# Optimization experiments

Hardware: AMD Instinct MI355X
Metric: run time of the kernel (lower is better)

## Reference

```python
import jax, jax.numpy as jnp
import numpy as np

# Dimensions: B sequences, T max length, K tagset size
B, T, K = 512, 512, 128
START_TAG_IDX, END_TAG_IDX = 126, 127
NEG = -10000.0  # matches torch.full(..., -10000)


def setup_inputs() -> dict:
    key = jax.random.key(0)
    k1, k2, k3 = jax.random.split(key, 3)
    feats = jax.random.normal(k1, (B, T, K), dtype=jnp.float32)
    trans = jax.random.normal(k2, (K, K), dtype=jnp.float32)
    # __init__ clamps illegal transitions: into START, out of END
    trans = trans.at[:, START_TAG_IDX].set(NEG)
    trans = trans.at[END_TAG_IDX, :].set(NEG)
    # pack_sequence requires length-descending order; lengths in [1, T]
    lengths = jnp.sort(jax.random.randint(k3, (B,), 1, T + 1))[::-1].astype(jnp.int32)
    return {"feats": feats, "trans": trans, "lengths": lengths}


def reference(feats, trans, lengths):
    # CRF log-partition (score_z): forward algorithm over a padded batch.
    # Equivalent to the packed-sequence loop: at step t only sequences with
    # t < length update alpha; others keep their previous alpha.
    Bq, Tq, Kq = feats.shape
    alpha0 = jnp.full((Bq, Kq), NEG, dtype=feats.dtype).at[:, START_TAG_IDX].set(0.0)
    feats_t = jnp.swapaxes(feats, 0, 1)                       # [T,B,K]
    mask = jnp.arange(Tq, dtype=lengths.dtype)[:, None] < lengths[None, :]  # [T,B]

    def step(alpha, inp):
        f, m = inp  # f: [B,K] emissions, m: [B] legal mask
        # score[b,i,j] = feat[b,j] + alpha[b,i] + trans[i,j]
        score = f[:, None, :] + alpha[:, :, None] + trans[None, :, :]  # [B,K,K]
        alpha_new = jax.nn.logsumexp(score, axis=1)                    # [B,K]
        return jnp.where(m[:, None], alpha_new, alpha), None

    alpha, _ = jax.lax.scan(step, alpha0, (feats_t, mask))
    final = alpha + trans[:, END_TAG_IDX][None, :]
    return jnp.sum(jax.nn.logsumexp(final, axis=1))
```

## Files before the change

### kernel.cpp

```cpp
#include <hip/hip_runtime.h>

#define K_TAGS 128
#define T_MAX  512
#define N_SEQ  512
#define START_TAG 126
#define END_TAG   127
#define LOG2E 1.44269504088896340736f
#define LN2   0.69314718055994530942f

typedef float v2f __attribute__((ext_vector_type(2)));

__device__ __forceinline__ float fexp2(float x) { return exp2f(x); }
__device__ __forceinline__ float flog2(float x) { return __log2f(x); }

template <int CTRL>
__device__ __forceinline__ float dpp_swap(float x) {
  return __int_as_float(__builtin_amdgcn_update_dpp(
      0, __float_as_int(x), CTRL, 0xF, 0xF, true));
}

__device__ __forceinline__ void lds_barrier() {
  asm volatile("s_waitcnt lgkmcnt(0)" ::: "memory");
  __builtin_amdgcn_s_barrier();
  asm volatile("" ::: "memory");
}

__global__ __launch_bounds__(256, 2) void crf_fwd_kernel(
    const float* __restrict__ feats,
    const float* __restrict__ trans,
    const int*   __restrict__ lengths,
    float*       __restrict__ partial)
{
  const int blk = blockIdx.x;
  const int b   = (blk < N_SEQ / 2) ? blk : (3 * N_SEQ / 2 - 1 - blk);
  const int tid = (int)threadIdx.x;
  const int jg  = tid >> 2;
  const int q   = tid & 3;
  const int j0  = jg;
  const int j1  = jg + 64;
  const int i0  = q * 32;

  const int len = lengths[b];
  const float* fb = feats + (size_t)b * (T_MAX * K_TAGS);

  __shared__ __align__(16) float p_sh[2][K_TAGS];
  __shared__ float nrm[2];
  __shared__ float red[8];

  v2f E0[16], E1[16];
#pragma unroll
  for (int c = 0; c < 8; ++c) {
    const int r = i0 + 4 * (c ^ (q << 1));
    E0[2 * c + 0] = v2f{fexp2(trans[(r + 0) * K_TAGS + j0] * LOG2E),
                        fexp2(trans[(r + 1) * K_TAGS + j0] * LOG2E)};
    E0[2 * c + 1] = v2f{fexp2(trans[(r + 2) * K_TAGS + j0] * LOG2E),
                        fexp2(trans[(r + 3) * K_TAGS + j0] * LOG2E)};
    E1[2 * c + 0] = v2f{fexp2(trans[(r + 0) * K_TAGS + j1] * LOG2E),
                        fexp2(trans[(r + 1) * K_TAGS + j1] * LOG2E)};
    E1[2 * c + 1] = v2f{fexp2(trans[(r + 2) * K_TAGS + j1] * LOG2E),
                        fexp2(trans[(r + 3) * K_TAGS + j1] * LOG2E)};
  }

  if (q == 0) {
    p_sh[0][j0] = (j0 == START_TAG) ? 1.0f : 0.0f;
    p_sh[0][j1] = (j1 == START_TAG) ? 1.0f : 0.0f;
  }
  if (tid == 0) nrm[0] = 0.0f;

  float a0 = (j0 == START_TAG) ? 0.0f : -10000.0f * LOG2E;
  float a1 = (j1 == START_TAG) ? 0.0f : -10000.0f * LOG2E;
  float Ncur = 0.0f;

  float f0cur = fb[j0];
  float f1cur = fb[j1];
  const int t1 = (len > 1) ? 1 : 0;
  float f0nx = fb[t1 * K_TAGS + j0];
  float f1nx = fb[t1 * K_TAGS + j1];

#define STEP(BUF, TT)                                                        \
  {                                                                          \
    const int tp = ((TT) + 2 < len) ? ((TT) + 2) : (len - 1);                \
    const float nf0 = fb[tp * K_TAGS + j0];                                  \
    const float nf1 = fb[tp * K_TAGS + j1];                                  \
    lds_barrier();                                                           \
    const float Nnxt = nrm[BUF];                                             \
    const float d  = Ncur - Nnxt;                                            \
    const float g0 = fexp2(fmaf(f0cur, LOG2E, d));                           \
    const float g1 = fexp2(fmaf(f1cur, LOG2E, d));                           \
    const float* pp = p_sh[BUF];                                             \
    v2f s0a = {0.f, 0.f}, s0b = {0.f, 0.f};                                  \
    v2f s1a = {0.f, 0.f}, s1b = {0.f, 0.f};                                  \
    _Pragma("unroll")                                                        \
    for (int c = 0; c < 8; ++c) {                                            \
      const int w0 = i0 + 4 * (c ^ (q << 1));                                \
      const float4 pv = *reinterpret_cast<const float4*>(pp + w0);           \
      const v2f pA = {pv.x, pv.y};                                           \
      const v2f pB = {pv.z, pv.w};                                           \
      s0a = __builtin_elementwise_fma(pA, E0[2 * c + 0], s0a);               \
      s0b = __builtin_elementwise_fma(pB, E0[2 * c + 1], s0b);               \
      s1a = __builtin_elementwise_fma(pA, E1[2 * c + 0], s1a);               \
      s1b = __builtin_elementwise_fma(pB, E1[2 * c + 1], s1b);               \
    }                                                                        \
    const v2f s0 = s0a + s0b;                                                \
    const v2f s1 = s1a + s1b;                                                \
    float acc0 = s0.x + s0.y;                                                \
    float acc1 = s1.x + s1.y;                                                \
    acc0 += dpp_swap<0xB1>(acc0);                                            \
    acc0 += dpp_swap<0x4E>(acc0);                                            \
    acc1 += dpp_swap<0xB1>(acc1);                                            \
    acc1 += dpp_swap<0x4E>(acc1);                                            \
    const float p0 = acc0 * g0;                                              \
    const float p1 = acc1 * g1;                                              \
    if (q < 2) p_sh[(BUF) ^ 1][(q == 0) ? j0 : j1] = (q == 0) ? p0 : p1;     \
    a0 = fmaf(f0cur, LOG2E, Ncur + flog2(acc0));                             \
    a1 = fmaf(f1cur, LOG2E, Ncur + flog2(acc1));                             \
    if (tid == 0) nrm[(BUF) ^ 1] = a0;                                       \
    Ncur = Nnxt;                                                             \
    f0cur = f0nx; f1cur = f1nx;                                              \
    f0nx = nf0;   f1nx = nf1;                                                \
  }

  int t = 0;
  for (; t + 2 <= len; t += 2) {
    STEP(0, t)
    STEP(1, t + 1)
  }
  if (t < len) STEP(0, t)
#undef STEP

  __syncthreads();

  const float fin0 = a0 + trans[j0 * K_TAGS + END_TAG] * LOG2E;
  const float fin1 = a1 + trans[j1 * K_TAGS + END_TAG] * LOG2E;

  float m = fmaxf(fin0, fin1);
#pragma unroll
  for (int off = 4; off < 64; off <<= 1)
    m = fmaxf(m, __shfl_xor(m, off, 64));
  if ((tid & 63) == 0) red[tid >> 6] = m;
  __syncthreads();
  const float Mf = fmaxf(fmaxf(red[0], red[1]), fmaxf(red[2], red[3]));

  float e = (q == 0) ? (fexp2(fin0 - Mf) + fexp2(fin1 - Mf)) : 0.0f;
#pragma unroll
  for (int off = 1; off < 64; off <<= 1)
    e += __shfl_xor(e, off, 64);
  if ((tid & 63) == 0) red[4 + (tid >> 6)] = e;
  __syncthreads();
  if (tid == 0) {
    const float s = (red[4] + red[5]) + (red[6] + red[7]);
    partial[b] = (Mf + flog2(s)) * LN2;
  }
}

__global__ void crf_reduce(const float* __restrict__ partial,
                           float* __restrict__ out) {
  const int tid = (int)threadIdx.x;
  float s = partial[tid] + partial[tid + 256];
#pragma unroll
  for (int off = 1; off < 64; off <<= 1) s += __shfl_xor(s, off, 64);
  __shared__ float ws[4];
  if ((tid & 63) == 0) ws[tid >> 6] = s;
  __syncthreads();
  if (tid == 0) out[0] = (ws[0] + ws[1]) + (ws[2] + ws[3]);
}

extern "C" void kernel_launch(void* const* d_in, const int* in_sizes, int n_in,
                              void* d_out, int out_size, void* d_ws, size_t ws_size,
                              hipStream_t stream) {
  const float* feats   = (const float*)d_in[0];
  const float* trans   = (const float*)d_in[1];
  const int*   lengths = (const int*)d_in[2];
  float* partial = (float*)d_ws;
  float* out     = (float*)d_out;

  crf_fwd_kernel<<<dim3(N_SEQ), dim3(256), 0, stream>>>(feats, trans, lengths, partial);
  crf_reduce<<<dim3(1), dim3(256), 0, stream>>>(partial, out);
}
```

Baseline: 335.7 us.

## Renormalize CRF probabilities every two steps via block max, drop per-step log

Replaces the per-step log-domain normalization, which computed a log2 of the accumulator and broadcast one alpha through LDS, with a probability-domain recurrence. The running probabilities are rescaled every other step by the block-wide max, gathered through a 16-entry LDS reduction, and the log of that scale is accumulated into a scalar. Feature prefetch is deepened to four steps, and raw amdgcn exp2/log builtins are used. This removes transcendentals and a dependency from the serial critical path, at the cost of relying on the values staying in float range across two unnormalized steps.

```diff
diff --git a/kernel.cpp b/kernel.cpp
--- a/kernel.cpp
+++ b/kernel.cpp
@@ -10,11 +10,23 @@
 
 typedef float v2f __attribute__((ext_vector_type(2)));
 
-__device__ __forceinline__ float fexp2(float x) { return exp2f(x); }
-__device__ __forceinline__ float flog2(float x) { return __log2f(x); }
+__device__ __forceinline__ float fexp2(float x) {
+#if __has_builtin(__builtin_amdgcn_exp2f)
+  return __builtin_amdgcn_exp2f(x);
+#else
+  return exp2f(x);
+#endif
+}
+__device__ __forceinline__ float flog2(float x) {
+#if __has_builtin(__builtin_amdgcn_logf)
+  return __builtin_amdgcn_logf(x);
+#else
+  return __log2f(x);
+#endif
+}
 
 template <int CTRL>
-__device__ __forceinline__ float dpp_swap(float x) {
+__device__ __forceinline__ float dpp_mov(float x) {
   return __int_as_float(__builtin_amdgcn_update_dpp(
       0, __float_as_int(x), CTRL, 0xF, 0xF, true));
 }
@@ -44,8 +56,8 @@
   const float* fb = feats + (size_t)b * (T_MAX * K_TAGS);
 
   __shared__ __align__(16) float p_sh[2][K_TAGS];
-  __shared__ float nrm[2];
-  __shared__ float red[8];
+  __shared__ __align__(16) float red16[16];
+  __shared__ float red8[8];
 
   v2f E0[16], E1[16];
 #pragma unroll
@@ -65,28 +77,41 @@
     p_sh[0][j0] = (j0 == START_TAG) ? 1.0f : 0.0f;
     p_sh[0][j1] = (j1 == START_TAG) ? 1.0f : 0.0f;
   }
-  if (tid == 0) nrm[0] = 0.0f;
-
-  float a0 = (j0 == START_TAG) ? 0.0f : -10000.0f * LOG2E;
-  float a1 = (j1 == START_TAG) ? 0.0f : -10000.0f * LOG2E;
-  float Ncur = 0.0f;
-
-  float f0cur = fb[j0];
-  float f1cur = fb[j1];
-  const int t1 = (len > 1) ? 1 : 0;
-  float f0nx = fb[t1 * K_TAGS + j0];
-  float f1nx = fb[t1 * K_TAGS + j1];
-
-#define STEP(BUF, TT)                                                        \
+
+  float Cc  = 0.0f;
+  float pc0 = 0.0f, pc1 = 0.0f;
+
+  float fA0, fA1, fB0, fB1, fC0, fC1, fD0, fD1;
+  {
+    const int tB = (len > 1) ? 1 : 0;
+    const int tC = (len > 2) ? 2 : (len - 1);
+    const int tD = (len > 3) ? 3 : (len - 1);
+    fA0 = fb[j0];                fA1 = fb[j1];
+    fB0 = fb[tB * K_TAGS + j0];  fB1 = fb[tB * K_TAGS + j1];
+    fC0 = fb[tC * K_TAGS + j0];  fC1 = fb[tC * K_TAGS + j1];
+    fD0 = fb[tD * K_TAGS + j0];  fD1 = fb[tD * K_TAGS + j1];
+  }
+
+#define BODY(BUF, F0, F1, ODD, TT)                                           \
   {                                                                          \
-    const int tp = ((TT) + 2 < len) ? ((TT) + 2) : (len - 1);                \
-    const float nf0 = fb[tp * K_TAGS + j0];                                  \
-    const float nf1 = fb[tp * K_TAGS + j1];                                  \
+    const float fl0 = F0, fl1 = F1;      \
+    const int tp = ((TT) + 4 < len) ? ((TT) + 4) : (len - 1);                \
+    F0 = fb[tp * K_TAGS + j0];    \
+    F1 = fb[tp * K_TAGS + j1];                                               \
     lds_barrier();                                                           \
-    const float Nnxt = nrm[BUF];                                             \
-    const float d  = Ncur - Nnxt;                                            \
-    const float g0 = fexp2(fmaf(f0cur, LOG2E, d));                           \
-    const float g1 = fexp2(fmaf(f1cur, LOG2E, d));                           \
+    float D = 0.0f;                                                          \
+    if (ODD) {     \
+      const float4 r0 = *reinterpret_cast<const float4*>(&red16[0]);         \
+      const float4 r1 = *reinterpret_cast<const float4*>(&red16[4]);         \
+      const float4 r2 = *reinterpret_cast<const float4*>(&red16[8]);         \
+      const float4 r3 = *reinterpret_cast<const float4*>(&red16[12]);        \
+      float mm = fmaxf(fmaxf(fmaxf(r0.x, r0.y), fmaxf(r0.z, r0.w)),          \
+                       fmaxf(fmaxf(r1.x, r1.y), fmaxf(r1.z, r1.w)));         \
+      mm = fmaxf(mm, fmaxf(fmaxf(fmaxf(r2.x, r2.y), fmaxf(r2.z, r2.w)),     \
+                           fmaxf(fmaxf(r3.x, r3.y), fmaxf(r3.z, r3.w))));   \
+      D = flog2(mm);                                                         \
+      Cc += D;                                                               \
+    }                                                                        \
     const float* pp = p_sh[BUF];                                             \
     v2f s0a = {0.f, 0.f}, s0b = {0.f, 0.f};                                  \
     v2f s1a = {0.f, 0.f}, s1b = {0.f, 0.f};                                  \
@@ -105,50 +130,55 @@
     const v2f s1 = s1a + s1b;                                                \
     float acc0 = s0.x + s0.y;                                                \
     float acc1 = s1.x + s1.y;                                                \
-    acc0 += dpp_swap<0xB1>(acc0);                                            \
-    acc0 += dpp_swap<0x4E>(acc0);                                            \
-    acc1 += dpp_swap<0xB1>(acc1);                                            \
-    acc1 += dpp_swap<0x4E>(acc1);                                            \
-    const float p0 = acc0 * g0;                                              \
-    const float p1 = acc1 * g1;                                              \
-    if (q < 2) p_sh[(BUF) ^ 1][(q == 0) ? j0 : j1] = (q == 0) ? p0 : p1;     \
-    a0 = fmaf(f0cur, LOG2E, Ncur + flog2(acc0));                             \
-    a1 = fmaf(f1cur, LOG2E, Ncur + flog2(acc1));                             \
-    if (tid == 0) nrm[(BUF) ^ 1] = a0;                                       \
-    Ncur = Nnxt;                                                             \
-    f0cur = f0nx; f1cur = f1nx;                                              \
-    f0nx = nf0;   f1nx = nf1;                                                \
+    acc0 += dpp_mov<0xB1>(acc0);                                             \
+    acc0 += dpp_mov<0x4E>(acc0);                                             \
+    acc1 += dpp_mov<0xB1>(acc1);                                             \
+    acc1 += dpp_mov<0x4E>(acc1);                                             \
+    const float g0 = fexp2(fmaf(fl0, LOG2E, -D));     \
+    const float g1 = fexp2(fmaf(fl1, LOG2E, -D));                            \
+    pc0 = acc0 * g0;                                                         \
+    pc1 = acc1 * g1;                                                         \
+    if (q < 2) p_sh[(BUF) ^ 1][(q == 0) ? j0 : j1] = (q == 0) ? pc0 : pc1;   \
+    if (!(ODD)) {      \
+      float mx = fmaxf(pc0, pc1);                                            \
+      mx = fmaxf(mx, dpp_mov<0x124>(mx));                                    \
+      mx = fmaxf(mx, dpp_mov<0x128>(mx));                                    \
+      if ((tid & 15) == 0) red16[tid >> 4] = mx;                             \
+    }                                                                        \
   }
 
   int t = 0;
-  for (; t + 2 <= len; t += 2) {
-    STEP(0, t)
-    STEP(1, t + 1)
-  }
-  if (t < len) STEP(0, t)
-#undef STEP
-
-  __syncthreads();
-
-  const float fin0 = a0 + trans[j0 * K_TAGS + END_TAG] * LOG2E;
-  const float fin1 = a1 + trans[j1 * K_TAGS + END_TAG] * LOG2E;
+  for (; t + 4 <= len; t += 4) {
+    BODY(0, fA0, fA1, 0, t)
+    BODY(1, fB0, fB1, 1, t + 1)
+    BODY(0, fC0, fC1, 0, t + 2)
+    BODY(1, fD0, fD1, 1, t + 3)
+  }
+  const int rem = len - t;
+  if (rem > 0) BODY(0, fA0, fA1, 0, t)
+  if (rem > 1) BODY(1, fB0, fB1, 1, t + 1)
+  if (rem > 2) BODY(0, fC0, fC1, 0, t + 2)
+#undef BODY
+
+  const float fin0 = flog2(pc0) + Cc + trans[j0 * K_TAGS + END_TAG] * LOG2E;
+  const float fin1 = flog2(pc1) + Cc + trans[j1 * K_TAGS + END_TAG] * LOG2E;
 
   float m = fmaxf(fin0, fin1);
 #pragma unroll
   for (int off = 4; off < 64; off <<= 1)
     m = fmaxf(m, __shfl_xor(m, off, 64));
-  if ((tid & 63) == 0) red[tid >> 6] = m;
+  if ((tid & 63) == 0) red8[tid >> 6] = m;
   __syncthreads();
-  const float Mf = fmaxf(fmaxf(red[0], red[1]), fmaxf(red[2], red[3]));
+  const float Mf = fmaxf(fmaxf(red8[0], red8[1]), fmaxf(red8[2], red8[3]));
 
   float e = (q == 0) ? (fexp2(fin0 - Mf) + fexp2(fin1 - Mf)) : 0.0f;
 #pragma unroll
   for (int off = 1; off < 64; off <<= 1)
     e += __shfl_xor(e, off, 64);
-  if ((tid & 63) == 0) red[4 + (tid >> 6)] = e;
+  if ((tid & 63) == 0) red8[4 + (tid >> 6)] = e;
   __syncthreads();
   if (tid == 0) {
-    const float s = (red[4] + red[5]) + (red[6] + red[7]);
+    const float s = (red8[4] + red8[5]) + (red8[6] + red8[7]);
     partial[b] = (Mf + flog2(s)) * LN2;
   }
 }
```

Result: faster. 324.8 us (-3.3%).
